# Kernel optimization log

Hardware: AMD Instinct MI355X
Metric: run time of the kernel (lower is better)

## Reference

```python
import jax, jax.numpy as jnp
import numpy as np

B, N, C = 4, 20480, 128
H, HD = 8, 16           # num_heads, head_dim (C // H)
L = 4                   # number of WindowBasedGraphAttentionBlocks
NW, WS = 320, 64        # num_windows, window_size (N // NW)
SCALE = HD ** -0.5
EPS = 1e-5


def layernorm(x, g, b):
    mu = jnp.mean(x, axis=-1, keepdims=True)
    var = jnp.mean(jnp.square(x - mu), axis=-1, keepdims=True)
    return (x - mu) * jax.lax.rsqrt(var + EPS) * g + b


def setup_inputs() -> dict:
    key = jax.random.key(0)
    ks = jax.random.split(key, 8)
    x = jax.random.normal(ks[0], (B, N, C), dtype=jnp.float32)
    # geodesic window mapping: each of NW windows has exactly WS members, permuted
    window_ids = jnp.asarray(
        np.random.RandomState(0).permutation(np.repeat(np.arange(NW), WS)),
        dtype=jnp.int32)
    s = 0.02
    inp = {
        'x': x,
        'g1': jnp.ones((L, C), jnp.float32),
        'be1': jnp.zeros((L, C), jnp.float32),
        'Wqkv': jax.random.normal(ks[1], (L, C, 3 * C), jnp.float32) * s,
        'bqkv': jnp.zeros((L, 3 * C), jnp.float32),
        'rel_bias': jax.random.normal(ks[2], (L, H, 1, 1), jnp.float32) * s,
        'Wproj': jax.random.normal(ks[3], (L, C, C), jnp.float32) * s,
        'bproj': jnp.zeros((L, C), jnp.float32),
        'g2': jnp.ones((L, C), jnp.float32),
        'be2': jnp.zeros((L, C), jnp.float32),
        'W1': jax.random.normal(ks[4], (L, C, 4 * C), jnp.float32) * s,
        'b1': jnp.zeros((L, 4 * C), jnp.float32),
        'W2': jax.random.normal(ks[5], (L, 4 * C, C), jnp.float32) * s,
        'b2': jnp.zeros((L, C), jnp.float32),
        'window_ids': window_ids,
    }
    return inp


def _encoder(x, g1, be1, Wqkv, bqkv, rel_bias, Wproj, bproj, g2, be2,
             W1, b1, W2, b2, sort_idx, inv_idx):
    def step(x, p):
        (g1, be1, Wqkv, bqkv, rb, Wp, bp, g2, be2, W1, b1, W2, b2) = p
        shortcut = x
        # GeodesicWindowPartition: gather by argsort(window_ids), split into windows
        win = x[:, sort_idx, :].reshape(B * NW, WS, C)
        h = layernorm(win, g1, be1)
        qkv = (h @ Wqkv + bqkv).reshape(B * NW, WS, 3, H, HD)
        q = qkv[:, :, 0].transpose(0, 2, 1, 3)  # [BW, H, WS, HD]
        k = qkv[:, :, 1].transpose(0, 2, 1, 3)
        v = qkv[:, :, 2].transpose(0, 2, 1, 3)
        attn = jnp.einsum('whqd,whkd->whqk', q, k) * SCALE
        attn = attn + rb[None]                  # relative geometry bias [H,1,1]
        attn = jax.nn.softmax(attn, axis=-1)
        out = jnp.einsum('whqk,whkd->whqd', attn, v)
        out = out.transpose(0, 2, 1, 3).reshape(B * NW, WS, C)
        out = out @ Wp + bp                     # AttentionOutputProjection
        rec = out.reshape(B, N, C)[:, inv_idx, :]  # partition.reverse
        x = shortcut + rec
        h2 = layernorm(x, g2, be2)
        x = x + (jax.nn.gelu(h2 @ W1 + b1) @ W2 + b2)
        return x, None

    params = (g1, be1, Wqkv, bqkv, rel_bias, Wproj, bproj, g2, be2, W1, b1, W2, b2)
    x, _ = jax.lax.scan(step, x, params)
    return x


def reference(x, g1, be1, Wqkv, bqkv, rel_bias, Wproj, bproj, g2, be2,
              W1, b1, W2, b2, window_ids):
    sort_idx = jnp.argsort(window_ids)
    inv_idx = jnp.argsort(sort_idx)
    return _encoder(x, g1, be1, Wqkv, bqkv, rel_bias, Wproj, bproj, g2, be2,
                    W1, b1, W2, b2, sort_idx, inv_idx)
```

## Files before the change

kernel.cpp:

```cpp
#include <hip/hip_runtime.h>
#include <hip/hip_bf16.h>
#include <math.h>

#define Nn 20480
#define Cc 128
#define Hh 8
#define Ll 4
#define NWw 320
#define BN 81920

typedef short sv8 __attribute__((ext_vector_type(8)));
typedef __bf16 bfv8 __attribute__((ext_vector_type(8)));
typedef float f32x4 __attribute__((ext_vector_type(4)));

__device__ __forceinline__ f32x4 mfma16(sv8 a, sv8 b, f32x4 c) {
    return __builtin_amdgcn_mfma_f32_16x16x32_bf16(
        __builtin_bit_cast(bfv8, a), __builtin_bit_cast(bfv8, b), c, 0, 0, 0);
}
__device__ __forceinline__ ushort f2bf(float f) {
    uint u = __float_as_uint(f);
    u += 0x7fffu + ((u >> 16) & 1u);
    return (ushort)(u >> 16);
}
__device__ __forceinline__ uint pk2bf(float lo, float hi) {
    uint r;
    asm("v_cvt_pk_bf16_f32 %0, %1, %2" : "=v"(r) : "v"(lo), "v"(hi));
    return r;
}
__device__ __forceinline__ float fast_gelu(float x) {
    float z = 0.7978845608f * (x + 0.044715f * x * x * x);
    return x * __builtin_amdgcn_rcpf(1.0f + __expf(-2.0f * z));
}

__global__ __launch_bounds__(64) void rank_kernel(const int* __restrict__ wid,
        int* __restrict__ lrank, int* __restrict__ hist) {
    __shared__ int keys[64];
    int c = blockIdx.x, lane = threadIdx.x;
    for (int j = lane; j < NWw; j += 64) hist[c * NWw + j] = 0;
    int i = c * 64 + lane;
    int w = wid[i];
    keys[lane] = w;
    __syncthreads();
    int rank = 0, total = 0;
    for (int j = 0; j < 64; ++j) {
        int kj = keys[j];
        total += (kj == w);
        rank += (j < lane && kj == w) ? 1 : 0;
    }
    lrank[i] = rank;
    if (rank == 0) hist[c * NWw + w] = total;
}
__global__ __launch_bounds__(64) void prefix_kernel(int* __restrict__ hist) {
    int w = blockIdx.x, lane = threadIdx.x;
    int running = 0;
    for (int it = 0; it < NWw / 64; ++it) {
        int c = it * 64 + lane;
        int v = hist[c * NWw + w];
        int orig = v;
        #pragma unroll
        for (int d = 1; d < 64; d <<= 1) {
            int tt = __shfl_up(v, d, 64);
            if (lane >= d) v += tt;
        }
        hist[c * NWw + w] = running + v - orig;
        running += __shfl(v, 63, 64);
    }
}
__global__ __launch_bounds__(64) void scatter_kernel(const int* __restrict__ wid,
        const int* __restrict__ lrank, const int* __restrict__ hist,
        int* __restrict__ sidx) {
    int c = blockIdx.x, lane = threadIdx.x;
    int i = c * 64 + lane;
    int w = wid[i];
    sidx[w * 64 + hist[c * NWw + w] + lrank[i]] = i;
}

__global__ __launch_bounds__(256) void wconv_kernel(
    const float* __restrict__ Wqkv, const float* __restrict__ Wproj,
    const float* __restrict__ W1, const float* __restrict__ W2,
    ushort* __restrict__ wt) {
    int id = blockIdx.x * 256 + threadIdx.x;
    int l = id / 196608;
    int r = id % 196608;
    const float* src; int dst;
    if (r < 49152) { int n = r % 384, k = r / 384;
        src = Wqkv + l * 49152 + k * 384 + n; dst = l * 196608 + n * 128 + k; }
    else if (r < 65536) { int rr = r - 49152; int n = rr % 128, k = rr / 128;
        src = Wproj + l * 16384 + k * 128 + n; dst = l * 196608 + 49152 + n * 128 + k; }
    else if (r < 131072) { int rr = r - 65536; int n = rr % 512, k = rr / 512;
        src = W1 + l * 65536 + k * 512 + n; dst = l * 196608 + 65536 + n * 128 + k; }
    else { int rr = r - 131072; int n = rr % 128, k = rr / 128;
        src = W2 + l * 65536 + k * 128 + n; dst = l * 196608 + 131072 + n * 512 + k; }
    wt[dst] = f2bf(*src);
}

__global__ __launch_bounds__(256, 2) void attn_fused_kernel(
    const float* __restrict__ xsrc, float* __restrict__ xdst,
    const ushort* __restrict__ wqkvT, const float* __restrict__ bqkv,
    const float* __restrict__ relb, const ushort* __restrict__ wprojT,
    const float* __restrict__ bproj, const float* __restrict__ g1,
    const float* __restrict__ be1, const int* __restrict__ sidx) {
    __shared__ __align__(16) ushort hl_[64][128];
    __shared__ __align__(16) ushort qkn[64][256];
    __shared__ __align__(16) ushort vT[128][76];
    __shared__ __align__(16) ushort pt[4][16][76];
    __shared__ int ridx[64];

    int t = threadIdx.x;
    int wave = t >> 6, lane = t & 63;
    int lr = lane & 15, lg = lane >> 4;
    int wb = blockIdx.x;
    int bN = (wb / NWw) * Nn;
    int p0 = (wb % NWw) * 64;

    if (t < 64) ridx[t] = sidx[p0 + t];
    __syncthreads();

    {
        int hl2 = lane & 31, hb = lane >> 5;
        float4 gg = *(const float4*)(g1 + hl2 * 4);
        float4 bb = *(const float4*)(be1 + hl2 * 4);
        #pragma unroll
        for (int it = 0; it < 8; ++it) {
            int row = it * 8 + wave * 2 + hb;
            int gi = bN + ridx[row];
            float4 v = *(const float4*)(xsrc + (size_t)gi * Cc + hl2 * 4);
            float s = v.x + v.y + v.z + v.w;
            s += __shfl_xor(s, 1, 64);  s += __shfl_xor(s, 2, 64);
            s += __shfl_xor(s, 4, 64);  s += __shfl_xor(s, 8, 64);
            s += __shfl_xor(s, 16, 64);
            float mu = s * 0.0078125f;
            float d0 = v.x - mu, d1 = v.y - mu, d2 = v.z - mu, d3 = v.w - mu;
            float q = d0 * d0 + d1 * d1 + d2 * d2 + d3 * d3;
            q += __shfl_xor(q, 1, 64);  q += __shfl_xor(q, 2, 64);
            q += __shfl_xor(q, 4, 64);  q += __shfl_xor(q, 8, 64);
            q += __shfl_xor(q, 16, 64);
            float rs = rsqrtf(q * 0.0078125f + 1e-5f);
            uint2 pk;
            pk.x = pk2bf(d0 * rs * gg.x + bb.x, d1 * rs * gg.y + bb.y);
            pk.y = pk2bf(d2 * rs * gg.z + bb.z, d3 * rs * gg.w + bb.w);
            *(uint2*)&hl_[row][(hl2 * 4) ^ ((row & 7) << 3)] = pk;
        }
    }
    __syncthreads();

    {
        f32x4 acc[4][6] = {};
        #pragma unroll
        for (int ks = 0; ks < 4; ++ks) {
            int k0 = ks * 32 + lg * 8;
            sv8 a[4], b[6];
            #pragma unroll
            for (int rf = 0; rf < 4; ++rf) {
                int row = rf * 16 + lr;
                a[rf] = *(const sv8*)&hl_[row][k0 ^ ((row & 7) << 3)];
            }
            #pragma unroll
            for (int nf = 0; nf < 6; ++nf) {
                int gcol = (nf < 2 ? 32 * wave + nf * 16
                          : nf < 4 ? 128 + 32 * wave + (nf - 2) * 16
                                   : 256 + 32 * wave + (nf - 4) * 16) + lr;
                b[nf] = *(const sv8*)(wqkvT + (size_t)gcol * 128 + k0);
            }
            #pragma unroll
            for (int rf = 0; rf < 4; ++rf)
                #pragma unroll
                for (int nf = 0; nf < 6; ++nf)
                    acc[rf][nf] = mfma16(a[rf], b[nf], acc[rf][nf]);
        }
        #pragma unroll
        for (int nf = 0; nf < 6; ++nf) {
            int gcol = (nf < 2 ? 32 * wave + nf * 16
                      : nf < 4 ? 128 + 32 * wave + (nf - 2) * 16
                               : 256 + 32 * wave + (nf - 4) * 16) + lr;
            float bs = bqkv[gcol];
            if (nf < 4) {
                #pragma unroll
                for (int rf = 0; rf < 4; ++rf)
                    #pragma unroll
                    for (int r = 0; r < 4; ++r) {
                        int row = rf * 16 + lg * 4 + r;
                        qkn[row][gcol ^ ((row & 7) << 3)] = f2bf(acc[rf][nf][r] + bs);
                    }
            } else {
                int dcol = gcol - 256;
                #pragma unroll
                for (int rf = 0; rf < 4; ++rf) {
                    uint2 pk;
                    pk.x = pk2bf(acc[rf][nf][0] + bs, acc[rf][nf][1] + bs);
                    pk.y = pk2bf(acc[rf][nf][2] + bs, acc[rf][nf][3] + bs);
                    *(uint2*)&vT[dcol][rf * 16 + lg * 4] = pk;
                }
            }
        }
    }
    __syncthreads();

    f32x4 zz = {0.f, 0.f, 0.f, 0.f};
    #pragma unroll
    for (int hi = 0; hi < 2; ++hi) {
        int hh = wave * 2 + hi;
        float rb = relb[hh];
        sv8 bv[2];
        #pragma unroll
        for (int ks = 0; ks < 2; ++ks)
            bv[ks] = *(const sv8*)&vT[hh * 16 + lr][ks * 32 + lg * 8];
        sv8 aq[4], bk[4];
        sv8 z = {0, 0, 0, 0, 0, 0, 0, 0};
        bool lo = (lg < 2);
        #pragma unroll
        for (int f = 0; f < 4; ++f) {
            aq[f] = z; bk[f] = z;
            if (lo) {
                int row = f * 16 + lr;
                aq[f] = *(const sv8*)&qkn[row][(hh * 16 + lg * 8) ^ ((row & 7) << 3)];
                bk[f] = *(const sv8*)&qkn[row][(128 + hh * 16 + lg * 8) ^ ((row & 7) << 3)];
            }
        }
        f32x4 s[4][4];
        #pragma unroll
        for (int kt = 0; kt < 4; ++kt)
            #pragma unroll
            for (int qt = 0; qt < 4; ++qt)
                s[kt][qt] = mfma16(bk[kt], aq[qt], zz);

        f32x4 o[4];
        #pragma unroll
        for (int qt = 0; qt < 4; ++qt) {
            float v[16];
            #pragma unroll
            for (int kt = 0; kt < 4; ++kt)
                #pragma unroll
                for (int r = 0; r < 4; ++r)
                    v[kt * 4 + r] = s[kt][qt][r] * 0.25f + rb;
            float m0 = fmaxf(fmaxf(fmaxf(v[0], v[1]), fmaxf(v[2], v[3])),
                             fmaxf(fmaxf(v[4], v[5]), fmaxf(v[6], v[7])));
            float m1 = fmaxf(fmaxf(fmaxf(v[8], v[9]), fmaxf(v[10], v[11])),
                             fmaxf(fmaxf(v[12], v[13]), fmaxf(v[14], v[15])));
            float mx = fmaxf(m0, m1);
            mx = fmaxf(mx, __shfl_xor(mx, 16, 64));
            mx = fmaxf(mx, __shfl_xor(mx, 32, 64));
            float sum = 0.f;
            #pragma unroll
            for (int i = 0; i < 16; ++i) {
                v[i] = __expf(v[i] - mx);
                sum += v[i];
            }
            sum += __shfl_xor(sum, 16, 64);
            sum += __shfl_xor(sum, 32, 64);
            float inv = __builtin_amdgcn_rcpf(sum);
            #pragma unroll
            for (int kt = 0; kt < 4; ++kt) {
                uint2 pk;
                pk.x = pk2bf(v[kt * 4 + 0] * inv, v[kt * 4 + 1] * inv);
                pk.y = pk2bf(v[kt * 4 + 2] * inv, v[kt * 4 + 3] * inv);
                *(uint2*)&pt[wave][lr][kt * 16 + lg * 4] = pk;
            }
            sv8 ap0 = *(const sv8*)&pt[wave][lr][lg * 8];
            sv8 ap1 = *(const sv8*)&pt[wave][lr][32 + lg * 8];
            o[qt] = mfma16(ap0, bv[0], zz);
            o[qt] = mfma16(ap1, bv[1], o[qt]);
        }
        #pragma unroll
        for (int qt = 0; qt < 4; ++qt)
            #pragma unroll
            for (int r = 0; r < 4; ++r) {
                int row = qt * 16 + lg * 4 + r;
                hl_[row][(hh * 16 + lr) ^ ((row & 7) << 3)] = f2bf(o[qt][r]);
            }
    }
    __syncthreads();

    {
        f32x4 acc[4][2] = {};
        #pragma unroll
        for (int ks = 0; ks < 4; ++ks) {
            int k0 = ks * 32 + lg * 8;
            sv8 a[4], b[2];
            #pragma unroll
            for (int rf = 0; rf < 4; ++rf) {
                int row = rf * 16 + lr;
                a[rf] = *(const sv8*)&hl_[row][k0 ^ ((row & 7) << 3)];
            }
            #pragma unroll
            for (int nf = 0; nf < 2; ++nf)
                b[nf] = *(const sv8*)(wprojT + (size_t)(wave * 32 + nf * 16 + lr) * 128 + k0);
            #pragma unroll
            for (int rf = 0; rf < 4; ++rf)
                #pragma unroll
                for (int nf = 0; nf < 2; ++nf)
                    acc[rf][nf] = mfma16(a[rf], b[nf], acc[rf][nf]);
        }
        #pragma unroll
        for (int nf = 0; nf < 2; ++nf) {
            int col = wave * 32 + nf * 16 + lr;
            float bs = bproj[col];
            #pragma unroll
            for (int rf = 0; rf < 4; ++rf)
                #pragma unroll
                for (int r = 0; r < 4; ++r) {
                    int row = rf * 16 + lg * 4 + r;
                    int gi = bN + ridx[row];
                    size_t ad = (size_t)gi * Cc + col;
                    xdst[ad] = xsrc[ad] + acc[rf][nf][r] + bs;
                }
        }
    }
}

__global__ __launch_bounds__(256, 2) void mlp_fused_kernel(
    const float* __restrict__ xsrc, float* __restrict__ xdst,
    const ushort* __restrict__ w1T, const float* __restrict__ b1,
    const ushort* __restrict__ w2T, const float* __restrict__ b2,
    const float* __restrict__ g2, const float* __restrict__ be2) {
    __shared__ __align__(16) ushort hl_[64][128];
    __shared__ __align__(16) ushort hid[64][512];
    int t = threadIdx.x, wave = t >> 6, lane = t & 63;
    int lr = lane & 15, lg = lane >> 4;
    int r0 = blockIdx.x * 64;

    {
        int hl2 = lane & 31, hb = lane >> 5;
        float4 gg = *(const float4*)(g2 + hl2 * 4);
        float4 bb = *(const float4*)(be2 + hl2 * 4);
        #pragma unroll
        for (int it = 0; it < 8; ++it) {
            int row = it * 8 + wave * 2 + hb;
            float4 v = *(const float4*)(xsrc + (size_t)(r0 + row) * Cc + hl2 * 4);
            float s = v.x + v.y + v.z + v.w;
            s += __shfl_xor(s, 1, 64);  s += __shfl_xor(s, 2, 64);
            s += __shfl_xor(s, 4, 64);  s += __shfl_xor(s, 8, 64);
            s += __shfl_xor(s, 16, 64);
            float mu = s * 0.0078125f;
            float d0 = v.x - mu, d1 = v.y - mu, d2 = v.z - mu, d3 = v.w - mu;
            float q = d0 * d0 + d1 * d1 + d2 * d2 + d3 * d3;
            q += __shfl_xor(q, 1, 64);  q += __shfl_xor(q, 2, 64);
            q += __shfl_xor(q, 4, 64);  q += __shfl_xor(q, 8, 64);
            q += __shfl_xor(q, 16, 64);
            float rs = rsqrtf(q * 0.0078125f + 1e-5f);
            uint2 pk;
            pk.x = pk2bf(d0 * rs * gg.x + bb.x, d1 * rs * gg.y + bb.y);
            pk.y = pk2bf(d2 * rs * gg.z + bb.z, d3 * rs * gg.w + bb.w);
            *(uint2*)&hl_[row][(hl2 * 4) ^ ((row & 7) << 3)] = pk;
        }
    }
    __syncthreads();

    {
        f32x4 acc[4][8] = {};
        #pragma unroll
        for (int ks = 0; ks < 4; ++ks) {
            int k0 = ks * 32 + lg * 8;
            sv8 a[4], b[8];
            #pragma unroll
            for (int rf = 0; rf < 4; ++rf) {
                int row = rf * 16 + lr;
                a[rf] = *(const sv8*)&hl_[row][k0 ^ ((row & 7) << 3)];
            }
            #pragma unroll
            for (int nf = 0; nf < 8; ++nf)
                b[nf] = *(const sv8*)(w1T + (size_t)(wave * 128 + nf * 16 + lr) * 128 + k0);
            #pragma unroll
            for (int rf = 0; rf < 4; ++rf)
                #pragma unroll
                for (int nf = 0; nf < 8; ++nf)
                    acc[rf][nf] = mfma16(a[rf], b[nf], acc[rf][nf]);
        }
        #pragma unroll
        for (int nf = 0; nf < 8; ++nf) {
            int col = wave * 128 + nf * 16 + lr;
            float bs = b1[col];
            #pragma unroll
            for (int rf = 0; rf < 4; ++rf)
                #pragma unroll
                for (int r = 0; r < 4; ++r) {
                    int row = rf * 16 + lg * 4 + r;
                    hid[row][col ^ ((row & 7) << 3)] = f2bf(fast_gelu(acc[rf][nf][r] + bs));
                }
        }
    }
    __syncthreads();

    {
        f32x4 acc2[4][2] = {};
        #pragma unroll
        for (int ks = 0; ks < 16; ++ks) {
            int k0 = ks * 32 + lg * 8;
            sv8 a[4], b[2];
            #pragma unroll
            for (int rf = 0; rf < 4; ++rf) {
                int row = rf * 16 + lr;
                a[rf] = *(const sv8*)&hid[row][k0 ^ ((row & 7) << 3)];
            }
            #pragma unroll
            for (int nf = 0; nf < 2; ++nf)
                b[nf] = *(const sv8*)(w2T + (size_t)(wave * 32 + nf * 16 + lr) * 512 + k0);
            #pragma unroll
            for (int rf = 0; rf < 4; ++rf)
                #pragma unroll
                for (int nf = 0; nf < 2; ++nf)
                    acc2[rf][nf] = mfma16(a[rf], b[nf], acc2[rf][nf]);
        }
        #pragma unroll
        for (int nf = 0; nf < 2; ++nf) {
            int col = wave * 32 + nf * 16 + lr;
            float bs = b2[col];
            #pragma unroll
            for (int rf = 0; rf < 4; ++rf)
                #pragma unroll
                for (int r = 0; r < 4; ++r) {
                    int row = rf * 16 + lg * 4 + r;
                    size_t ad = (size_t)(r0 + row) * Cc + col;
                    xdst[ad] = xsrc[ad] + acc2[rf][nf][r] + bs;
                }
        }
    }
}

extern "C" void kernel_launch(void* const* d_in, const int* in_sizes, int n_in,
                              void* d_out, int out_size, void* d_ws, size_t ws_size,
                              hipStream_t stream) {
    const float* x_in   = (const float*)d_in[0];
    const float* g1     = (const float*)d_in[1];
    const float* be1    = (const float*)d_in[2];
    const float* Wqkv   = (const float*)d_in[3];
    const float* bqkv   = (const float*)d_in[4];
    const float* relb   = (const float*)d_in[5];
    const float* Wproj  = (const float*)d_in[6];
    const float* bproj  = (const float*)d_in[7];
    const float* g2     = (const float*)d_in[8];
    const float* be2    = (const float*)d_in[9];
    const float* W1     = (const float*)d_in[10];
    const float* b1     = (const float*)d_in[11];
    const float* W2     = (const float*)d_in[12];
    const float* b2     = (const float*)d_in[13];
    const int*   wid    = (const int*)d_in[14];

    size_t off = 0;
    float* x_ws = (float*)d_ws;                      off += (size_t)BN * Cc * 4;
    ushort* wt  = (ushort*)((char*)d_ws + off);      off += (size_t)786432 * 2;
    int* sidx   = (int*)((char*)d_ws + off);         off += (size_t)Nn * 4;
    int* lrank  = (int*)((char*)d_ws + off);         off += (size_t)Nn * 4;
    int* hist   = (int*)((char*)d_ws + off);         off += (size_t)NWw * NWw * 4;
    if (ws_size < off) return;

    rank_kernel<<<Nn / 64, 64, 0, stream>>>(wid, lrank, hist);
    prefix_kernel<<<NWw, 64, 0, stream>>>(hist);
    scatter_kernel<<<Nn / 64, 64, 0, stream>>>(wid, lrank, hist, sidx);
    wconv_kernel<<<786432 / 256, 256, 0, stream>>>(Wqkv, Wproj, W1, W2, wt);

    for (int l = 0; l < Ll; ++l) {
        const ushort* wqkvT  = wt + (size_t)l * 196608;
        const ushort* wprojT = wqkvT + 49152;
        const ushort* w1T    = wqkvT + 65536;
        const ushort* w2T    = wqkvT + 131072;
        const float* xsrc = (l == 0) ? x_in : x_ws;

        attn_fused_kernel<<<BN / 64, 256, 0, stream>>>(
            xsrc, x_ws, wqkvT, bqkv + l * 384, relb + l * Hh,
            wprojT, bproj + l * Cc, g1 + l * Cc, be1 + l * Cc, sidx);

        float* xdst = (l == Ll - 1) ? (float*)d_out : x_ws;
        mlp_fused_kernel<<<BN / 64, 256, 0, stream>>>(
            x_ws, xdst, w1T, b1 + l * 512, w2T, b2 + l * Cc,
            g2 + l * Cc, be2 + l * Cc);
    }
}
```

Baseline: 456.3 us.

## Fuse attention and MLP blocks into a single per-layer kernel

Merges the attention kernel and the MLP kernel into one kernel per layer. The post-attention residual stays in registers and feeds LayerNorm2 directly, and the MLP output is scattered back through the window permutation. This removes one full write and read of the activation tensor per layer, plus one launch. Shared memory is reused through an arena, and the first MLP GEMM is split into two halves to limit register pressure. LayerNorm2 now uses a one-pass E[x²]−μ² variance, which carries a small numerical risk.

```diff
diff --git a/kernel.cpp b/kernel.cpp
--- a/kernel.cpp
+++ b/kernel.cpp
@@ -94,17 +94,23 @@
     wt[dst] = f2bf(*src);
 }
 
-__global__ __launch_bounds__(256, 2) void attn_fused_kernel(
+__global__ __launch_bounds__(256, 2) void layer_fused_kernel(
     const float* __restrict__ xsrc, float* __restrict__ xdst,
     const ushort* __restrict__ wqkvT, const float* __restrict__ bqkv,
     const float* __restrict__ relb, const ushort* __restrict__ wprojT,
     const float* __restrict__ bproj, const float* __restrict__ g1,
-    const float* __restrict__ be1, const int* __restrict__ sidx) {
+    const float* __restrict__ be1, const float* __restrict__ g2,
+    const float* __restrict__ be2, const ushort* __restrict__ w1T,
+    const float* __restrict__ b1, const ushort* __restrict__ w2T,
+    const float* __restrict__ b2, const int* __restrict__ sidx) {
     __shared__ __align__(16) ushort hl_[64][128];
-    __shared__ __align__(16) ushort qkn[64][256];
-    __shared__ __align__(16) ushort vT[128][76];
-    __shared__ __align__(16) ushort pt[4][16][76];
-    __shared__ int ridx[64];
+    __shared__ __align__(16) char arenaB[65536];
+    ushort* qkn = (ushort*)arenaB;
+    ushort* vT  = (ushort*)(arenaB + 32768);
+    ushort* pt  = (ushort*)(arenaB + 51200);
+    int*   ridx = (int*)(arenaB + 60928);
+    float* redbuf = (float*)arenaB;
+    ushort (*hid)[512] = (ushort (*)[512])arenaB;
 
     int t = threadIdx.x;
     int wave = t >> 6, lane = t & 63;
@@ -180,7 +186,7 @@
                     #pragma unroll
                     for (int r = 0; r < 4; ++r) {
                         int row = rf * 16 + lg * 4 + r;
-                        qkn[row][gcol ^ ((row & 7) << 3)] = f2bf(acc[rf][nf][r] + bs);
+                        qkn[row * 256 + (gcol ^ ((row & 7) << 3))] = f2bf(acc[rf][nf][r] + bs);
                     }
             } else {
                 int dcol = gcol - 256;
@@ -189,7 +195,7 @@
                     uint2 pk;
                     pk.x = pk2bf(acc[rf][nf][0] + bs, acc[rf][nf][1] + bs);
                     pk.y = pk2bf(acc[rf][nf][2] + bs, acc[rf][nf][3] + bs);
-                    *(uint2*)&vT[dcol][rf * 16 + lg * 4] = pk;
+                    *(uint2*)&vT[dcol * 72 + rf * 16 + lg * 4] = pk;
                 }
             }
         }
@@ -204,7 +210,7 @@
         sv8 bv[2];
         #pragma unroll
         for (int ks = 0; ks < 2; ++ks)
-            bv[ks] = *(const sv8*)&vT[hh * 16 + lr][ks * 32 + lg * 8];
+            bv[ks] = *(const sv8*)&vT[(hh * 16 + lr) * 72 + ks * 32 + lg * 8];
         sv8 aq[4], bk[4];
         sv8 z = {0, 0, 0, 0, 0, 0, 0, 0};
         bool lo = (lg < 2);
@@ -213,8 +219,8 @@
             aq[f] = z; bk[f] = z;
             if (lo) {
                 int row = f * 16 + lr;
-                aq[f] = *(const sv8*)&qkn[row][(hh * 16 + lg * 8) ^ ((row & 7) << 3)];
-                bk[f] = *(const sv8*)&qkn[row][(128 + hh * 16 + lg * 8) ^ ((row & 7) << 3)];
+                aq[f] = *(const sv8*)&qkn[row * 256 + ((hh * 16 + lg * 8) ^ ((row & 7) << 3))];
+                bk[f] = *(const sv8*)&qkn[row * 256 + ((128 + hh * 16 + lg * 8) ^ ((row & 7) << 3))];
             }
         }
         f32x4 s[4][4];
@@ -225,6 +231,7 @@
                 s[kt][qt] = mfma16(bk[kt], aq[qt], zz);
 
         f32x4 o[4];
+        ushort* ptw = pt + wave * 16 * 76;
         #pragma unroll
         for (int qt = 0; qt < 4; ++qt) {
             float v[16];
@@ -254,10 +261,10 @@
                 uint2 pk;
                 pk.x = pk2bf(v[kt * 4 + 0] * inv, v[kt * 4 + 1] * inv);
                 pk.y = pk2bf(v[kt * 4 + 2] * inv, v[kt * 4 + 3] * inv);
-                *(uint2*)&pt[wave][lr][kt * 16 + lg * 4] = pk;
-            }
-            sv8 ap0 = *(const sv8*)&pt[wave][lr][lg * 8];
-            sv8 ap1 = *(const sv8*)&pt[wave][lr][32 + lg * 8];
+                *(uint2*)&ptw[lr * 76 + kt * 16 + lg * 4] = pk;
+            }
+            sv8 ap0 = *(const sv8*)&ptw[lr * 76 + lg * 8];
+            sv8 ap1 = *(const sv8*)&ptw[lr * 76 + 32 + lg * 8];
             o[qt] = mfma16(ap0, bv[0], zz);
             o[qt] = mfma16(ap1, bv[1], o[qt]);
         }
@@ -271,8 +278,8 @@
     }
     __syncthreads();
 
-    {
-        f32x4 acc[4][2] = {};
+    f32x4 acc_x[4][2] = {};
+    {
         #pragma unroll
         for (int ks = 0; ks < 4; ++ks) {
             int k0 = ks * 32 + lg * 8;
@@ -289,7 +296,7 @@
             for (int rf = 0; rf < 4; ++rf)
                 #pragma unroll
                 for (int nf = 0; nf < 2; ++nf)
-                    acc[rf][nf] = mfma16(a[rf], b[nf], acc[rf][nf]);
+                    acc_x[rf][nf] = mfma16(a[rf], b[nf], acc_x[rf][nf]);
         }
         #pragma unroll
         for (int nf = 0; nf < 2; ++nf) {
@@ -301,74 +308,83 @@
                 for (int r = 0; r < 4; ++r) {
                     int row = rf * 16 + lg * 4 + r;
                     int gi = bN + ridx[row];
-                    size_t ad = (size_t)gi * Cc + col;
-                    xdst[ad] = xsrc[ad] + acc[rf][nf][r] + bs;
-                }
-        }
-    }
-}
-
-__global__ __launch_bounds__(256, 2) void mlp_fused_kernel(
-    const float* __restrict__ xsrc, float* __restrict__ xdst,
-    const ushort* __restrict__ w1T, const float* __restrict__ b1,
-    const ushort* __restrict__ w2T, const float* __restrict__ b2,
-    const float* __restrict__ g2, const float* __restrict__ be2) {
-    __shared__ __align__(16) ushort hl_[64][128];
-    __shared__ __align__(16) ushort hid[64][512];
-    int t = threadIdx.x, wave = t >> 6, lane = t & 63;
-    int lr = lane & 15, lg = lane >> 4;
-    int r0 = blockIdx.x * 64;
-
-    {
-        int hl2 = lane & 31, hb = lane >> 5;
-        float4 gg = *(const float4*)(g2 + hl2 * 4);
-        float4 bb = *(const float4*)(be2 + hl2 * 4);
-        #pragma unroll
-        for (int it = 0; it < 8; ++it) {
-            int row = it * 8 + wave * 2 + hb;
-            float4 v = *(const float4*)(xsrc + (size_t)(r0 + row) * Cc + hl2 * 4);
-            float s = v.x + v.y + v.z + v.w;
-            s += __shfl_xor(s, 1, 64);  s += __shfl_xor(s, 2, 64);
-            s += __shfl_xor(s, 4, 64);  s += __shfl_xor(s, 8, 64);
-            s += __shfl_xor(s, 16, 64);
-            float mu = s * 0.0078125f;
-            float d0 = v.x - mu, d1 = v.y - mu, d2 = v.z - mu, d3 = v.w - mu;
-            float q = d0 * d0 + d1 * d1 + d2 * d2 + d3 * d3;
-            q += __shfl_xor(q, 1, 64);  q += __shfl_xor(q, 2, 64);
-            q += __shfl_xor(q, 4, 64);  q += __shfl_xor(q, 8, 64);
-            q += __shfl_xor(q, 16, 64);
-            float rs = rsqrtf(q * 0.0078125f + 1e-5f);
-            uint2 pk;
-            pk.x = pk2bf(d0 * rs * gg.x + bb.x, d1 * rs * gg.y + bb.y);
-            pk.y = pk2bf(d2 * rs * gg.z + bb.z, d3 * rs * gg.w + bb.w);
-            *(uint2*)&hl_[row][(hl2 * 4) ^ ((row & 7) << 3)] = pk;
-        }
-    }
-    __syncthreads();
-
-    {
-        f32x4 acc[4][8] = {};
+                    acc_x[rf][nf][r] += xsrc[(size_t)gi * Cc + col] + bs;
+                }
+        }
+    }
+    {
+        #pragma unroll
+        for (int rf = 0; rf < 4; ++rf)
+            #pragma unroll
+            for (int r = 0; r < 4; ++r) {
+                float s = acc_x[rf][0][r] + acc_x[rf][1][r];
+                float q = acc_x[rf][0][r] * acc_x[rf][0][r] + acc_x[rf][1][r] * acc_x[rf][1][r];
+                s += __shfl_xor(s, 1, 64);  q += __shfl_xor(q, 1, 64);
+                s += __shfl_xor(s, 2, 64);  q += __shfl_xor(q, 2, 64);
+                s += __shfl_xor(s, 4, 64);  q += __shfl_xor(q, 4, 64);
+                s += __shfl_xor(s, 8, 64);  q += __shfl_xor(q, 8, 64);
+                if (lr == 0) {
+                    int row = rf * 16 + lg * 4 + r;
+                    redbuf[(row * 4 + wave) * 2 + 0] = s;
+                    redbuf[(row * 4 + wave) * 2 + 1] = q;
+                }
+            }
+    }
+    __syncthreads();
+    {
+        float g2a[2], be2a[2];
+        #pragma unroll
+        for (int nf = 0; nf < 2; ++nf) {
+            int col = wave * 32 + nf * 16 + lr;
+            g2a[nf] = g2[col];
+            be2a[nf] = be2[col];
+        }
+        #pragma unroll
+        for (int rf = 0; rf < 4; ++rf)
+            #pragma unroll
+            for (int r = 0; r < 4; ++r) {
+                int row = rf * 16 + lg * 4 + r;
+                float s = redbuf[(row * 4 + 0) * 2] + redbuf[(row * 4 + 1) * 2]
+                        + redbuf[(row * 4 + 2) * 2] + redbuf[(row * 4 + 3) * 2];
+                float q = redbuf[(row * 4 + 0) * 2 + 1] + redbuf[(row * 4 + 1) * 2 + 1]
+                        + redbuf[(row * 4 + 2) * 2 + 1] + redbuf[(row * 4 + 3) * 2 + 1];
+                float mu = s * 0.0078125f;
+                float var = q * 0.0078125f - mu * mu;
+                float rs = rsqrtf(var + 1e-5f);
+                #pragma unroll
+                for (int nf = 0; nf < 2; ++nf) {
+                    int col = wave * 32 + nf * 16 + lr;
+                    float xh = (acc_x[rf][nf][r] - mu) * rs * g2a[nf] + be2a[nf];
+                    hl_[row][col ^ ((row & 7) << 3)] = f2bf(xh);
+                }
+            }
+    }
+    __syncthreads();
+
+    #pragma unroll
+    for (int hf2 = 0; hf2 < 2; ++hf2) {
+        f32x4 acc[4][4] = {};
         #pragma unroll
         for (int ks = 0; ks < 4; ++ks) {
             int k0 = ks * 32 + lg * 8;
-            sv8 a[4], b[8];
+            sv8 a[4], b[4];
             #pragma unroll
             for (int rf = 0; rf < 4; ++rf) {
                 int row = rf * 16 + lr;
                 a[rf] = *(const sv8*)&hl_[row][k0 ^ ((row & 7) << 3)];
             }
             #pragma unroll
-            for (int nf = 0; nf < 8; ++nf)
-                b[nf] = *(const sv8*)(w1T + (size_t)(wave * 128 + nf * 16 + lr) * 128 + k0);
-            #pragma unroll
-            for (int rf = 0; rf < 4; ++rf)
-                #pragma unroll
-                for (int nf = 0; nf < 8; ++nf)
+            for (int nf = 0; nf < 4; ++nf)
+                b[nf] = *(const sv8*)(w1T + (size_t)(wave * 128 + hf2 * 64 + nf * 16 + lr) * 128 + k0);
+            #pragma unroll
+            for (int rf = 0; rf < 4; ++rf)
+                #pragma unroll
+                for (int nf = 0; nf < 4; ++nf)
                     acc[rf][nf] = mfma16(a[rf], b[nf], acc[rf][nf]);
         }
         #pragma unroll
-        for (int nf = 0; nf < 8; ++nf) {
-            int col = wave * 128 + nf * 16 + lr;
+        for (int nf = 0; nf < 4; ++nf) {
+            int col = wave * 128 + hf2 * 64 + nf * 16 + lr;
             float bs = b1[col];
             #pragma unroll
             for (int rf = 0; rf < 4; ++rf)
@@ -410,8 +426,8 @@
                 #pragma unroll
                 for (int r = 0; r < 4; ++r) {
                     int row = rf * 16 + lg * 4 + r;
-                    size_t ad = (size_t)(r0 + row) * Cc + col;
-                    xdst[ad] = xsrc[ad] + acc2[rf][nf][r] + bs;
+                    int gi = bN + sidx[p0 + row];
+                    xdst[(size_t)gi * Cc + col] = acc_x[rf][nf][r] + acc2[rf][nf][r] + bs;
                 }
         }
     }
@@ -455,14 +471,12 @@
         const ushort* w1T    = wqkvT + 65536;
         const ushort* w2T    = wqkvT + 131072;
         const float* xsrc = (l == 0) ? x_in : x_ws;
-
-        attn_fused_kernel<<<BN / 64, 256, 0, stream>>>(
-            xsrc, x_ws, wqkvT, bqkv + l * 384, relb + l * Hh,
-            wprojT, bproj + l * Cc, g1 + l * Cc, be1 + l * Cc, sidx);
-
         float* xdst = (l == Ll - 1) ? (float*)d_out : x_ws;
-        mlp_fused_kernel<<<BN / 64, 256, 0, stream>>>(
-            x_ws, xdst, w1T, b1 + l * 512, w2T, b2 + l * Cc,
-            g2 + l * Cc, be2 + l * Cc);
-    }
-}
+
+        layer_fused_kernel<<<BN / 64, 256, 0, stream>>>(
+            xsrc, xdst, wqkvT, bqkv + l * 384, relb + l * Hh,
+            wprojT, bproj + l * Cc, g1 + l * Cc, be1 + l * Cc,
+            g2 + l * Cc, be2 + l * Cc, w1T, b1 + l * 512,
+            w2T, b2 + l * Cc, sidx);
+    }
+}
```

Result: no change. 461.1 us (+1.1%).

## Restructure MLP kernel into 128-row tiles with chunked hidden dim and LDS-staged weights

Applied to the files above, without the earlier changes.

The fused MLP kernel now processes 128 rows per block and walks the 512-wide hidden dimension in 8 chunks of 64. Each chunk's W1 and W2 slices are staged into swizzled LDS, with the next chunk prefetched into registers while the current one is computed. The second GEMM accumulates across chunks in registers. This replaces per-wave direct global loads of weights and the full 64x512 hidden buffer, aiming to reuse weights across more rows and cut global weight traffic. The cost is more barriers per block, fewer blocks, and higher register pressure from the prefetch buffer and accumulators.

```diff
diff --git a/kernel.cpp b/kernel.cpp
--- a/kernel.cpp
+++ b/kernel.cpp
@@ -308,23 +308,26 @@
     }
 }
 
-__global__ __launch_bounds__(256, 2) void mlp_fused_kernel(
+__global__ __launch_bounds__(256, 2) void mlp128_kernel(
     const float* __restrict__ xsrc, float* __restrict__ xdst,
     const ushort* __restrict__ w1T, const float* __restrict__ b1,
     const ushort* __restrict__ w2T, const float* __restrict__ b2,
     const float* __restrict__ g2, const float* __restrict__ be2) {
-    __shared__ __align__(16) ushort hl_[64][128];
-    __shared__ __align__(16) ushort hid[64][512];
+    __shared__ __align__(16) ushort h_[128][128];
+    __shared__ __align__(16) char w1c[16384];
+    __shared__ __align__(16) char w2c[16384];
+    __shared__ __align__(16) ushort hid[128][64];
     int t = threadIdx.x, wave = t >> 6, lane = t & 63;
     int lr = lane & 15, lg = lane >> 4;
-    int r0 = blockIdx.x * 64;
+    int mw = wave >> 1, nw = wave & 1;
+    int r0 = blockIdx.x * 128;
 
     {
         int hl2 = lane & 31, hb = lane >> 5;
         float4 gg = *(const float4*)(g2 + hl2 * 4);
         float4 bb = *(const float4*)(be2 + hl2 * 4);
         #pragma unroll
-        for (int it = 0; it < 8; ++it) {
+        for (int it = 0; it < 16; ++it) {
             int row = it * 8 + wave * 2 + hb;
             float4 v = *(const float4*)(xsrc + (size_t)(r0 + row) * Cc + hl2 * 4);
             float s = v.x + v.y + v.z + v.w;
@@ -341,79 +344,116 @@
             uint2 pk;
             pk.x = pk2bf(d0 * rs * gg.x + bb.x, d1 * rs * gg.y + bb.y);
             pk.y = pk2bf(d2 * rs * gg.z + bb.z, d3 * rs * gg.w + bb.w);
-            *(uint2*)&hl_[row][(hl2 * 4) ^ ((row & 7) << 3)] = pk;
-        }
-    }
-    __syncthreads();
-
+            *(uint2*)&h_[row][(hl2 * 4) ^ ((row & 7) << 3)] = pk;
+        }
+    }
+
+    uint4 wreg[8];
     {
-        f32x4 acc[4][8] = {};
-        #pragma unroll
-        for (int ks = 0; ks < 4; ++ks) {
-            int k0 = ks * 32 + lg * 8;
-            sv8 a[4], b[8];
+        #pragma unroll
+        for (int j = 0; j < 4; ++j) {
+            int off = j * 4096 + wave * 1024 + lane * 16;
+            wreg[j] = *(const uint4*)((const char*)w1T + off);
+            int off2 = j * 4096 + wave * 1024 + lane * 16;
+            int n = off2 >> 7, kb = off2 & 127;
+            wreg[4 + j] = *(const uint4*)((const char*)w2T + (size_t)n * 1024 + kb);
+        }
+    }
+
+    f32x4 acc2[4][4] = {};
+    for (int c = 0; c < 8; ++c) {
+        __syncthreads();
+        #pragma unroll
+        for (int j = 0; j < 4; ++j) {
+            int off = j * 4096 + wave * 1024 + lane * 16;
+            int n = off >> 8, kb = off & 255;
+            *(uint4*)(w1c + n * 256 + (kb ^ ((n & 7) << 4))) = wreg[j];
+            int n2 = off >> 7, kb2 = off & 127;
+            *(uint4*)(w2c + n2 * 128 + (kb2 ^ ((n2 & 7) << 4))) = wreg[4 + j];
+        }
+        if (c < 7) {
+            const char* p1 = (const char*)w1T + (c + 1) * 16384;
+            #pragma unroll
+            for (int j = 0; j < 4; ++j) {
+                int off = j * 4096 + wave * 1024 + lane * 16;
+                wreg[j] = *(const uint4*)(p1 + off);
+                int n = off >> 7, kb = off & 127;
+                wreg[4 + j] = *(const uint4*)((const char*)w2T + (size_t)n * 1024 + (c + 1) * 128 + kb);
+            }
+        }
+        __syncthreads();
+
+        {
+            f32x4 acc[4][2] = {};
+            #pragma unroll
+            for (int ks = 0; ks < 4; ++ks) {
+                int kB = ks * 64 + lg * 16;
+                sv8 a[4], b[2];
+                #pragma unroll
+                for (int rf = 0; rf < 4; ++rf) {
+                    int row = mw * 64 + rf * 16 + lr;
+                    a[rf] = *(const sv8*)&h_[row][(ks * 32 + lg * 8) ^ ((row & 7) << 3)];
+                }
+                #pragma unroll
+                for (int nf = 0; nf < 2; ++nf) {
+                    int n = nw * 32 + nf * 16 + lr;
+                    b[nf] = *(const sv8*)(w1c + n * 256 + (kB ^ ((n & 7) << 4)));
+                }
+                #pragma unroll
+                for (int rf = 0; rf < 4; ++rf)
+                    #pragma unroll
+                    for (int nf = 0; nf < 2; ++nf)
+                        acc[rf][nf] = mfma16(a[rf], b[nf], acc[rf][nf]);
+            }
+            #pragma unroll
+            for (int nf = 0; nf < 2; ++nf) {
+                int lcol = nw * 32 + nf * 16 + lr;
+                float bs = b1[c * 64 + lcol];
+                #pragma unroll
+                for (int rf = 0; rf < 4; ++rf)
+                    #pragma unroll
+                    for (int r = 0; r < 4; ++r) {
+                        int row = mw * 64 + rf * 16 + lg * 4 + r;
+                        hid[row][lcol ^ ((row & 7) << 3)] = f2bf(fast_gelu(acc[rf][nf][r] + bs));
+                    }
+            }
+        }
+        __syncthreads();
+
+        #pragma unroll
+        for (int ks = 0; ks < 2; ++ks) {
+            int kB = ks * 64 + lg * 16;
+            sv8 a[4], b[4];
             #pragma unroll
             for (int rf = 0; rf < 4; ++rf) {
-                int row = rf * 16 + lr;
-                a[rf] = *(const sv8*)&hl_[row][k0 ^ ((row & 7) << 3)];
-            }
-            #pragma unroll
-            for (int nf = 0; nf < 8; ++nf)
-                b[nf] = *(const sv8*)(w1T + (size_t)(wave * 128 + nf * 16 + lr) * 128 + k0);
+                int row = mw * 64 + rf * 16 + lr;
+                a[rf] = *(const sv8*)&hid[row][(ks * 32 + lg * 8) ^ ((row & 7) << 3)];
+            }
+            #pragma unroll
+            for (int nf = 0; nf < 4; ++nf) {
+                int n = nw * 64 + nf * 16 + lr;
+                b[nf] = *(const sv8*)(w2c + n * 128 + (kB ^ ((n & 7) << 4)));
+            }
             #pragma unroll
             for (int rf = 0; rf < 4; ++rf)
                 #pragma unroll
-                for (int nf = 0; nf < 8; ++nf)
-                    acc[rf][nf] = mfma16(a[rf], b[nf], acc[rf][nf]);
-        }
-        #pragma unroll
-        for (int nf = 0; nf < 8; ++nf) {
-            int col = wave * 128 + nf * 16 + lr;
-            float bs = b1[col];
-            #pragma unroll
-            for (int rf = 0; rf < 4; ++rf)
-                #pragma unroll
-                for (int r = 0; r < 4; ++r) {
-                    int row = rf * 16 + lg * 4 + r;
-                    hid[row][col ^ ((row & 7) << 3)] = f2bf(fast_gelu(acc[rf][nf][r] + bs));
-                }
-        }
-    }
-    __syncthreads();
-
-    {
-        f32x4 acc2[4][2] = {};
-        #pragma unroll
-        for (int ks = 0; ks < 16; ++ks) {
-            int k0 = ks * 32 + lg * 8;
-            sv8 a[4], b[2];
-            #pragma unroll
-            for (int rf = 0; rf < 4; ++rf) {
-                int row = rf * 16 + lr;
-                a[rf] = *(const sv8*)&hid[row][k0 ^ ((row & 7) << 3)];
-            }
-            #pragma unroll
-            for (int nf = 0; nf < 2; ++nf)
-                b[nf] = *(const sv8*)(w2T + (size_t)(wave * 32 + nf * 16 + lr) * 512 + k0);
-            #pragma unroll
-            for (int rf = 0; rf < 4; ++rf)
-                #pragma unroll
-                for (int nf = 0; nf < 2; ++nf)
+                for (int nf = 0; nf < 4; ++nf)
                     acc2[rf][nf] = mfma16(a[rf], b[nf], acc2[rf][nf]);
         }
-        #pragma unroll
-        for (int nf = 0; nf < 2; ++nf) {
-            int col = wave * 32 + nf * 16 + lr;
-            float bs = b2[col];
-            #pragma unroll
-            for (int rf = 0; rf < 4; ++rf)
-                #pragma unroll
-                for (int r = 0; r < 4; ++r) {
-                    int row = rf * 16 + lg * 4 + r;
-                    size_t ad = (size_t)(r0 + row) * Cc + col;
-                    xdst[ad] = xsrc[ad] + acc2[rf][nf][r] + bs;
-                }
-        }
+    }
+
+    #pragma unroll
+    for (int nf = 0; nf < 4; ++nf) {
+        int col = nw * 64 + nf * 16 + lr;
+        float bs = b2[col];
+        #pragma unroll
+        for (int rf = 0; rf < 4; ++rf)
+            #pragma unroll
+            for (int r = 0; r < 4; ++r) {
+                int row = r0 + mw * 64 + rf * 16 + lg * 4 + r;
+                size_t ad = (size_t)row * Cc + col;
+                xdst[ad] = xsrc[ad] + acc2[rf][nf][r] + bs;
+            }
     }
 }
 
@@ -461,7 +501,7 @@
             wprojT, bproj + l * Cc, g1 + l * Cc, be1 + l * Cc, sidx);
 
         float* xdst = (l == Ll - 1) ? (float*)d_out : x_ws;
-        mlp_fused_kernel<<<BN / 64, 256, 0, stream>>>(
+        mlp128_kernel<<<BN / 128, 256, 0, stream>>>(
             x_ws, xdst, w1T, b1 + l * 512, w2T, b2 + l * Cc,
             g2 + l * Cc, be2 + l * Cc);
     }
```

Measured after the change: 569.1 us. 1.25x slower.
